# Performance work log

Hardware: AMD Instinct MI355X
Metric: run time of the kernel (lower is better)

Reference implementation:

```python
import jax, jax.numpy as jnp
import numpy as np

DIM = 768
HEADS = 12
HEAD_DIM = DIM // HEADS
HIDDEN = 4 * DIM


def layer_norm(x, g, b, eps=1e-5):
    mu = jnp.mean(x, axis=-1, keepdims=True)
    var = jnp.var(x, axis=-1, keepdims=True)
    return (x - mu) * jax.lax.rsqrt(var + eps) * g + b


def setup_inputs() -> dict:
    key = jax.random.key(0)
    ks = jax.random.split(key, 8)
    s = lambda fan_in: 1.0 / np.sqrt(fan_in)
    return {
        "x": jax.random.normal(ks[0], (16, 577, DIM), dtype=jnp.float32),
        "ln1_g": jnp.ones((DIM,), jnp.float32),
        "ln1_b": jnp.zeros((DIM,), jnp.float32),
        "w_qkv": jax.random.uniform(ks[1], (DIM, 3 * DIM), jnp.float32, -s(DIM), s(DIM)),
        "b_qkv": jnp.zeros((3 * DIM,), jnp.float32),
        "w_proj": jax.random.uniform(ks[2], (DIM, DIM), jnp.float32, -s(DIM), s(DIM)),
        "b_proj": jnp.zeros((DIM,), jnp.float32),
        "ln2_g": jnp.ones((DIM,), jnp.float32),
        "ln2_b": jnp.zeros((DIM,), jnp.float32),
        "w_fc1": jax.random.uniform(ks[3], (DIM, HIDDEN), jnp.float32, -s(DIM), s(DIM)),
        "b_fc1": jnp.zeros((HIDDEN,), jnp.float32),
        "w_fc2": jax.random.uniform(ks[4], (HIDDEN, DIM), jnp.float32, -s(HIDDEN), s(HIDDEN)),
        "b_fc2": jnp.zeros((DIM,), jnp.float32),
    }


def reference(x, ln1_g, ln1_b, w_qkv, b_qkv, w_proj, b_proj,
              ln2_g, ln2_b, w_fc1, b_fc1, w_fc2, b_fc2):
    B, N, C = x.shape
    scale = HEAD_DIM ** -0.5

    # --- attention branch (pre-norm) ---
    h = layer_norm(x, ln1_g, ln1_b)
    qkv = h @ w_qkv + b_qkv                               # [B,N,3C]
    qkv = qkv.reshape(B, N, 3, HEADS, HEAD_DIM)
    q, k, v = [qkv[:, :, i].transpose(0, 2, 1, 3) for i in range(3)]  # [B,H,N,D]
    attn = jnp.einsum("bhnd,bhmd->bhnm", q, k) * scale
    attn = jax.nn.softmax(attn, axis=-1)
    out = jnp.einsum("bhnm,bhmd->bhnd", attn, v)          # [B,H,N,D]
    out = out.transpose(0, 2, 1, 3).reshape(B, N, C)
    x = x + (out @ w_proj + b_proj)

    # --- MLP branch (pre-norm) ---
    h = layer_norm(x, ln2_g, ln2_b)
    h = jax.nn.gelu(h @ w_fc1 + b_fc1, approximate=False)
    x = x + (h @ w_fc2 + b_fc2)
    return x
```

## Files before the change

### kernel.cpp

```cpp
#include <hip/hip_runtime.h>
#include <hip/hip_bf16.h>
#include <math.h>

#define NB   16
#define NTOK 577
#define CDIM 768
#define NH   12
#define HID  3072
#define RTOT (NB*NTOK)
#define RPAD (((RTOT+127)/128)*128)
#define BH   (NB*NH)
#define QT   40
#define KF_C (CDIM/32)

typedef __attribute__((ext_vector_type(8))) short bf16x8;
typedef __attribute__((ext_vector_type(4))) float f32x4;
typedef unsigned short u16;

__device__ inline void load_lds16(const void* g, void* l) {
    __builtin_amdgcn_global_load_lds(
        (const __attribute__((address_space(1))) unsigned*)g,
        (__attribute__((address_space(3))) unsigned*)l, 16, 0, 0);
}

__device__ inline size_t blobA(int m, int c, int Kf) {
    return ((size_t)(m >> 4) * Kf + (c >> 5)) * 512 +
           (((c >> 3) & 3) * 16 + (m & 15)) * 8 + (c & 7);
}

__device__ inline float fast_gelu(float x) {
    float y = 0.7978845608f * (x + 0.044715f * x * x * x);
    float e = __expf(2.0f * y);
    float th = 1.0f - 2.0f / (e + 1.0f);
    return 0.5f * x * (1.0f + th);
}

__global__ __launch_bounds__(256) void wconvert_blob(
    const float* __restrict__ src, u16* __restrict__ dst, int K, int N)
{
    int n  = blockIdx.x * 256 + threadIdx.x;
    int kp = blockIdx.y;
    const float* s = src + (size_t)(kp * 8) * N + n;
    __hip_bfloat16 h0 = __float2bfloat16(s[0 * N]);
    __hip_bfloat16 h1 = __float2bfloat16(s[1 * N]);
    __hip_bfloat16 h2 = __float2bfloat16(s[2 * N]);
    __hip_bfloat16 h3 = __float2bfloat16(s[3 * N]);
    __hip_bfloat16 h4 = __float2bfloat16(s[4 * N]);
    __hip_bfloat16 h5 = __float2bfloat16(s[5 * N]);
    __hip_bfloat16 h6 = __float2bfloat16(s[6 * N]);
    __hip_bfloat16 h7 = __float2bfloat16(s[7 * N]);
    ushort4 a = make_ushort4(*(u16*)&h0, *(u16*)&h1, *(u16*)&h2, *(u16*)&h3);
    ushort4 b = make_ushort4(*(u16*)&h4, *(u16*)&h5, *(u16*)&h6, *(u16*)&h7);
    u16* d = dst + ((size_t)(n >> 4) * (K >> 5) + (kp >> 2)) * 512 +
             ((kp & 3) * 16 + (n & 15)) * 8;
    *(ushort4*)(d)     = a;
    *(ushort4*)(d + 4) = b;
}

__global__ __launch_bounds__(256) void ln_kernel(
    const float* __restrict__ x, const float* __restrict__ g,
    const float* __restrict__ b, u16* __restrict__ out)
{
    int row = blockIdx.x;
    const float* xr = x + (size_t)row * CDIM;
    int t = threadIdx.x;
    float v0 = xr[t], v1 = xr[t + 256], v2 = xr[t + 512];
    float s  = v0 + v1 + v2;
    float s2 = v0*v0 + v1*v1 + v2*v2;
    #pragma unroll
    for (int off = 32; off; off >>= 1) {
        s  += __shfl_xor(s, off);
        s2 += __shfl_xor(s2, off);
    }
    __shared__ float red[10];
    int wave = t >> 6, lane = t & 63;
    if (lane == 0) { red[wave] = s; red[wave + 4] = s2; }
    __syncthreads();
    if (t == 0) {
        float ts  = red[0] + red[1] + red[2] + red[3];
        float ts2 = red[4] + red[5] + red[6] + red[7];
        float mu  = ts * (1.0f / CDIM);
        float var = ts2 * (1.0f / CDIM) - mu * mu;
        red[8] = mu;
        red[9] = rsqrtf(var + 1e-5f);
    }
    __syncthreads();
    float mu = red[8], rs = red[9];
    #pragma unroll
    for (int i = 0; i < 3; ++i) {
        int c = t + i * 256;
        float v = (i == 0 ? v0 : (i == 1 ? v1 : v2));
        __hip_bfloat16 hb = __float2bfloat16((v - mu) * rs * g[c] + b[c]);
        out[blobA(row, c, KF_C)] = *(u16*)&hb;
    }
}

template<int TM>
__global__ __launch_bounds__(64) void flat_gemm(
    const u16* __restrict__ Ab, const u16* __restrict__ Bb,
    const float* __restrict__ bias, const float* __restrict__ res,
    void* __restrict__ outv,
    u16* __restrict__ Qp, u16* __restrict__ Kp, u16* __restrict__ Vp,
    int M, int Nc, int K, int nb, int mb, int flags)
{
    __shared__ u16 sb[TM * 1024];
    int lane = threadIdx.x & 63;
    int fr = lane & 15, fq = lane >> 4;

    int fid = blockIdx.x;
    int xcd = fid & 7, w = fid >> 3;
    int slab = w / nb, n = w - slab * nb;
    int m = slab * 8 + xcd;
    if (m >= mb) return;
    int m0 = m * (TM * 16), n0 = n * 64;

    int Kf = K >> 5;
    size_t tstr = (size_t)Kf * 512;
    const u16* Ap = Ab + (size_t)(m0 >> 4) * tstr + lane * 8;
    const u16* Bp = Bb + (size_t)(n0 >> 4) * tstr + lane * 8;

    f32x4 acc[TM][4];
    #pragma unroll
    for (int i = 0; i < TM; ++i)
        #pragma unroll
        for (int j = 0; j < 4; ++j) acc[i][j] = (f32x4){0.f, 0.f, 0.f, 0.f};

    bf16x8 af[TM], bf[4];
    #pragma unroll
    for (int tm = 0; tm < TM; ++tm) af[tm] = *(const bf16x8*)(Ap + tm * tstr);
    #pragma unroll
    for (int tn = 0; tn < 4; ++tn) bf[tn] = *(const bf16x8*)(Bp + tn * tstr);

    for (int kf = 0; kf < Kf; ++kf) {
        bf16x8 an[TM], bn[4];
        if (kf + 1 < Kf) {
            size_t o = (size_t)(kf + 1) * 512;
            #pragma unroll
            for (int tm = 0; tm < TM; ++tm)
                an[tm] = *(const bf16x8*)(Ap + tm * tstr + o);
            #pragma unroll
            for (int tn = 0; tn < 4; ++tn)
                bn[tn] = *(const bf16x8*)(Bp + tn * tstr + o);
        }
        #pragma unroll
        for (int tm = 0; tm < TM; ++tm)
            #pragma unroll
            for (int tn = 0; tn < 4; ++tn)
                acc[tm][tn] = __builtin_amdgcn_mfma_f32_16x16x32_bf16(
                    af[tm], bf[tn], acc[tm][tn], 0, 0, 0);
        #pragma unroll
        for (int i = 0; i < TM; ++i) af[i] = an[i];
        #pragma unroll
        for (int i = 0; i < 4; ++i)  bf[i] = bn[i];
    }

    float* outf = (float*)outv;
    u16* outblob = (u16*)outv;
    int gelu = flags & 1;
    int KfO = Nc >> 5;

    if (flags & 8) {
        int sec = n0 / CDIM;
        int h   = (n0 % CDIM) / 64;
        #pragma unroll
        for (int tm = 0; tm < TM; ++tm) {
            #pragma unroll
            for (int rg = 0; rg < 4; ++rg) {
                int gm = m0 + tm * 16 + fq * 4 + rg;
                if (gm >= M) continue;
                int b   = gm / NTOK;
                int row = gm - b * NTOK;
                int bh  = b * NH + h;
                #pragma unroll
                for (int tn = 0; tn < 4; ++tn) {
                    int d = tn * 16 + fr;
                    float v = acc[tm][tn][rg] + bias[n0 + tn * 16 + fr];
                    __hip_bfloat16 hb = __float2bfloat16(v);
                    if (sec == 0) {
                        Qp[(size_t)(bh * QT + (row >> 4)) * 1024 + (d >> 5) * 512 +
                           (((d >> 3) & 3) * 16 + (row & 15)) * 8 + (d & 7)] = *(u16*)&hb;
                    } else if (sec == 1) {
                        Kp[(size_t)(bh * QT + (row >> 4)) * 1024 + (d >> 5) * 512 +
                           (((d >> 3) & 3) * 16 + (row & 15)) * 8 + (d & 7)] = *(u16*)&hb;
                    } else {
                        Vp[((size_t)(bh * 4 + (d >> 4)) * 20 + (row >> 5)) * 512 +
                           (((row >> 3) & 3) * 16 + (d & 15)) * 8 + (row & 7)] = *(u16*)&hb;
                    }
                }
            }
        }
        return;
    }

    if (flags & 4) {
        #pragma unroll
        for (int tm = 0; tm < TM; ++tm)
            #pragma unroll
            for (int tn = 0; tn < 4; ++tn)
                #pragma unroll
                for (int rg = 0; rg < 4; ++rg) {
                    int cl = tn * 16 + fr;
                    float v = acc[tm][tn][rg] + bias[n0 + cl];
                    if (gelu) v = fast_gelu(v);
                    __hip_bfloat16 hb = __float2bfloat16(v);
                    sb[tm * 1024 + (cl >> 5) * 512 +
                       (((cl >> 3) & 3) * 16 + fq * 4 + rg) * 8 + (cl & 7)] = *(u16*)&hb;
                }
        #pragma unroll
        for (int tm = 0; tm < TM; ++tm) {
            u16* dst = outblob + ((size_t)((m0 >> 4) + tm) * KfO + (n0 >> 5)) * 512;
            *(bf16x8*)(dst + lane * 16)     = *(const bf16x8*)(sb + tm * 1024 + lane * 16);
            *(bf16x8*)(dst + lane * 16 + 8) = *(const bf16x8*)(sb + tm * 1024 + lane * 16 + 8);
        }
        return;
    }

    #pragma unroll
    for (int tm = 0; tm < TM; ++tm) {
        #pragma unroll
        for (int rg = 0; rg < 4; ++rg) {
            int gm = m0 + tm * 16 + fq * 4 + rg;
            if (gm >= M) continue;
            #pragma unroll
            for (int tn = 0; tn < 4; ++tn) {
                int gn = n0 + tn * 16 + fr;
                float v = acc[tm][tn][rg] + bias[gn];
                if (gelu) v = fast_gelu(v);
                if (res)  v += res[(size_t)gm * Nc + gn];
                outf[(size_t)gm * Nc + gn] = v;
            }
        }
    }
}

__global__ __launch_bounds__(256) void attn_mfma(
    const u16* __restrict__ Qp, const u16* __restrict__ Kp,
    const u16* __restrict__ Vp, u16* __restrict__ outp)
{
    __shared__ __align__(16) u16 Ks[4096];
    __shared__ __align__(16) u16 Vs[4096];
    __shared__ __align__(16) u16 Ps[4 * 16 * 72];

    int bh = blockIdx.y, qc = blockIdx.x;
    int b = bh / NH, h = bh % NH;
    int t = threadIdx.x, lane = t & 63, wv = t >> 6;
    int fr = lane & 15, fq = lane >> 4;

    int mt = qc * 4 + wv;
    const u16* qbase = Qp + (size_t)(bh * QT + mt) * 1024 + lane * 8;
    bf16x8 qf0 = *(const bf16x8*)(qbase);
    bf16x8 qf1 = *(const bf16x8*)(qbase + 512);

    const u16* kg = Kp + (size_t)bh * (QT * 1024) + wv * 1024 + lane * 8;
    const u16* vg = Vp + ((size_t)(bh * 4 + wv) * 20) * 512 + lane * 8;
    u16* lK  = Ks + wv * 1024;
    u16* lV  = Vs + wv * 1024;
    u16* psw = Ps + wv * (16 * 72);

    f32x4 o[4];
    float m_r[4], l_r[4];
    #pragma unroll
    for (int i = 0; i < 4; ++i) {
        o[i] = (f32x4){0.f, 0.f, 0.f, 0.f};
        m_r[i] = -1e30f; l_r[i] = 0.f;
    }

    for (int kt = 0; kt < 10; ++kt) {
        load_lds16(kg + kt * 4096,       lK);
        load_lds16(kg + kt * 4096 + 512, lK + 512);
        load_lds16(vg + kt * 1024,       lV);
        load_lds16(vg + kt * 1024 + 512, lV + 512);
        __syncthreads();

        f32x4 sc[4];
        #pragma unroll
        for (int nt = 0; nt < 4; ++nt) {
            sc[nt] = (f32x4){0.f, 0.f, 0.f, 0.f};
            bf16x8 kf0 = *(const bf16x8*)(Ks + (nt * 2 + 0) * 512 + lane * 8);
            bf16x8 kf1 = *(const bf16x8*)(Ks + (nt * 2 + 1) * 512 + lane * 8);
            sc[nt] = __builtin_amdgcn_mfma_f32_16x16x32_bf16(qf0, kf0, sc[nt], 0, 0, 0);
            sc[nt] = __builtin_amdgcn_mfma_f32_16x16x32_bf16(qf1, kf1, sc[nt], 0, 0, 0);
        }

        int j0 = kt * 64;
        float p[4][4], rm[4];
        #pragma unroll
        for (int rg = 0; rg < 4; ++rg) rm[rg] = -1e30f;
        #pragma unroll
        for (int nt = 0; nt < 4; ++nt) {
            bool valid = (j0 + nt * 16 + fr) < NTOK;
            #pragma unroll
            for (int rg = 0; rg < 4; ++rg) {
                float sv = valid ? sc[nt][rg] * 0.125f : -1e30f;
                p[nt][rg] = sv;
                rm[rg] = fmaxf(rm[rg], sv);
            }
        }
        #pragma unroll
        for (int rg = 0; rg < 4; ++rg) {
            #pragma unroll
            for (int off = 1; off < 16; off <<= 1)
                rm[rg] = fmaxf(rm[rg], __shfl_xor(rm[rg], off));
        }
        float alpha[4], rs[4];
        #pragma unroll
        for (int rg = 0; rg < 4; ++rg) {
            float mn = fmaxf(m_r[rg], rm[rg]);
            alpha[rg] = __expf(m_r[rg] - mn);
            m_r[rg] = mn;
            rs[rg] = 0.f;
        }
        #pragma unroll
        for (int nt = 0; nt < 4; ++nt)
            #pragma unroll
            for (int rg = 0; rg < 4; ++rg) {
                float pv = __expf(p[nt][rg] - m_r[rg]);
                p[nt][rg] = pv;
                rs[rg] += pv;
            }
        #pragma unroll
        for (int rg = 0; rg < 4; ++rg) {
            #pragma unroll
            for (int off = 1; off < 16; off <<= 1)
                rs[rg] += __shfl_xor(rs[rg], off);
            l_r[rg] = l_r[rg] * alpha[rg] + rs[rg];
        }

        #pragma unroll
        for (int nt = 0; nt < 4; ++nt)
            #pragma unroll
            for (int rg = 0; rg < 4; ++rg) {
                __hip_bfloat16 hb = __float2bfloat16(p[nt][rg]);
                psw[(fq * 4 + rg) * 72 + nt * 16 + fr] = *(u16*)&hb;
            }
        #pragma unroll
        for (int dt = 0; dt < 4; ++dt)
            #pragma unroll
            for (int rg = 0; rg < 4; ++rg)
                o[dt][rg] *= alpha[rg];

        bf16x8 pf0 = *(const bf16x8*)(psw + fr * 72 + fq * 8);
        bf16x8 pf1 = *(const bf16x8*)(psw + fr * 72 + 32 + fq * 8);
        #pragma unroll
        for (int dt = 0; dt < 4; ++dt) {
            bf16x8 bv0 = *(const bf16x8*)(Vs + (dt * 2 + 0) * 512 + lane * 8);
            bf16x8 bv1 = *(const bf16x8*)(Vs + (dt * 2 + 1) * 512 + lane * 8);
            o[dt] = __builtin_amdgcn_mfma_f32_16x16x32_bf16(pf0, bv0, o[dt], 0, 0, 0);
            o[dt] = __builtin_amdgcn_mfma_f32_16x16x32_bf16(pf1, bv1, o[dt], 0, 0, 0);
        }
        __syncthreads();
    }

    #pragma unroll
    for (int rg = 0; rg < 4; ++rg) {
        int row = qc * 64 + wv * 16 + fq * 4 + rg;
        if (row < NTOK) {
            float rl = 1.0f / l_r[rg];
            int grow = b * NTOK + row;
            #pragma unroll
            for (int dt = 0; dt < 4; ++dt) {
                __hip_bfloat16 hb = __float2bfloat16(o[dt][rg] * rl);
                outp[blobA(grow, h * 64 + dt * 16 + fr, KF_C)] = *(u16*)&hb;
            }
        }
    }
}

static inline int swz_grid(int nb, int mb) { return nb * (((mb + 7) / 8) * 8); }

extern "C" void kernel_launch(void* const* d_in, const int* in_sizes, int n_in,
                              void* d_out, int out_size, void* d_ws, size_t ws_size,
                              hipStream_t stream)
{
    const float* x      = (const float*)d_in[0];
    const float* ln1_g  = (const float*)d_in[1];
    const float* ln1_b  = (const float*)d_in[2];
    const float* w_qkv  = (const float*)d_in[3];
    const float* b_qkv  = (const float*)d_in[4];
    const float* w_proj = (const float*)d_in[5];
    const float* b_proj = (const float*)d_in[6];
    const float* ln2_g  = (const float*)d_in[7];
    const float* ln2_b  = (const float*)d_in[8];
    const float* w_fc1  = (const float*)d_in[9];
    const float* b_fc1  = (const float*)d_in[10];
    const float* w_fc2  = (const float*)d_in[11];
    const float* b_fc2  = (const float*)d_in[12];
    float* out = (float*)d_out;

    char* w = (char*)d_ws;
    u16* Bqkv = (u16*)w; w += (size_t)3*CDIM*CDIM*2;
    u16* Bproj= (u16*)w; w += (size_t)CDIM*CDIM*2;
    u16* Bfc1 = (u16*)w; w += (size_t)HID*CDIM*2;
    u16* Bfc2 = (u16*)w; w += (size_t)CDIM*HID*2;
    u16* hA   = (u16*)w; w += (size_t)RPAD*CDIM*2;
    u16* h3A  = (u16*)w; w += (size_t)RPAD*HID*2;
    u16* Qp   = (u16*)w; w += (size_t)BH*QT*1024*2;
    u16* Kp   = (u16*)w; w += (size_t)BH*QT*1024*2;
    u16* Vp   = (u16*)w; w += (size_t)BH*4*20*512*2;

    int mb4 = (RTOT + 63) / 64;

    wconvert_blob<<<dim3(3*CDIM/256, CDIM/8), 256, 0, stream>>>(w_qkv,  Bqkv, CDIM, 3*CDIM);
    wconvert_blob<<<dim3(CDIM/256,   CDIM/8), 256, 0, stream>>>(w_proj, Bproj, CDIM, CDIM);
    wconvert_blob<<<dim3(HID/256,    CDIM/8), 256, 0, stream>>>(w_fc1,  Bfc1, CDIM, HID);
    wconvert_blob<<<dim3(CDIM/256,   HID/8),  256, 0, stream>>>(w_fc2,  Bfc2, HID, CDIM);

    ln_kernel<<<RTOT, 256, 0, stream>>>(x, ln1_g, ln1_b, hA);
    flat_gemm<4><<<swz_grid(3*CDIM/64, mb4), 64, 0, stream>>>(
        hA, Bqkv, b_qkv, nullptr, nullptr, Qp, Kp, Vp,
        RTOT, 3*CDIM, CDIM, 3*CDIM/64, mb4, 8);
    attn_mfma<<<dim3(10, BH), 256, 0, stream>>>(Qp, Kp, Vp, hA);
    flat_gemm<4><<<swz_grid(CDIM/64, mb4), 64, 0, stream>>>(
        hA, Bproj, b_proj, x, out, nullptr, nullptr, nullptr,
        RTOT, CDIM, CDIM, CDIM/64, mb4, 0);
    ln_kernel<<<RTOT, 256, 0, stream>>>(out, ln2_g, ln2_b, hA);
    flat_gemm<4><<<swz_grid(HID/64, mb4), 64, 0, stream>>>(
        hA, Bfc1, b_fc1, nullptr, h3A, nullptr, nullptr, nullptr,
        RTOT, HID, CDIM, HID/64, mb4, 1 | 4);
    flat_gemm<4><<<swz_grid(CDIM/64, mb4), 64, 0, stream>>>(
        h3A, Bfc2, b_fc2, out, out, nullptr, nullptr, nullptr,
        RTOT, CDIM, HID, CDIM/64, mb4, 0);
}
```

Baseline: 486.0 us.

## Replace single-wave register GEMM with 4-wave LDS-staged double-buffered tile GEMM

Replaces the one-wavefront GEMM that streamed A and B fragments straight from global memory into registers with a 256-thread kernel. Each block stages a larger tile (128x128 or 64x128) into LDS via global_load_lds with double buffering, and four waves share it as a 2x2 layout. This raises reuse of loaded A/B data across waves and cuts redundant global traffic. The cost is a block-wide barrier per K step and no XCD-aware block swizzle. Flags become template parameters, and the gelu branch in the fp32 epilogue is dropped.

```diff
diff --git a/kernel.cpp b/kernel.cpp
--- a/kernel.cpp
+++ b/kernel.cpp
@@ -95,86 +95,92 @@
     }
 }
 
-template<int TM>
-__global__ __launch_bounds__(64) void flat_gemm(
+template<int MBL, int NBL, int FLAGS>
+__global__ __launch_bounds__(256) void tile_gemm(
     const u16* __restrict__ Ab, const u16* __restrict__ Bb,
     const float* __restrict__ bias, const float* __restrict__ res,
     void* __restrict__ outv,
     u16* __restrict__ Qp, u16* __restrict__ Kp, u16* __restrict__ Vp,
-    int M, int Nc, int K, int nb, int mb, int flags)
+    int M, int Nc, int K)
 {
-    __shared__ u16 sb[TM * 1024];
-    int lane = threadIdx.x & 63;
+    constexpr int NST  = (MBL + NBL) / 4;
+    constexpr int BUFU = (MBL + NBL) * 512;
+    constexpr int MH2  = MBL / 2, NW2 = NBL / 2;
+    __shared__ __align__(16) u16 smem[2 * BUFU];
+
+    int tid = threadIdx.x, lane = tid & 63, wv = tid >> 6;
     int fr = lane & 15, fq = lane >> 4;
-
-    int fid = blockIdx.x;
-    int xcd = fid & 7, w = fid >> 3;
-    int slab = w / nb, n = w - slab * nb;
-    int m = slab * 8 + xcd;
-    if (m >= mb) return;
-    int m0 = m * (TM * 16), n0 = n * 64;
-
+    int wm = wv >> 1, wn = wv & 1;
+
+    int m0 = blockIdx.y * (MBL * 16), n0 = blockIdx.x * (NBL * 16);
     int Kf = K >> 5;
     size_t tstr = (size_t)Kf * 512;
-    const u16* Ap = Ab + (size_t)(m0 >> 4) * tstr + lane * 8;
-    const u16* Bp = Bb + (size_t)(n0 >> 4) * tstr + lane * 8;
-
-    f32x4 acc[TM][4];
-    #pragma unroll
-    for (int i = 0; i < TM; ++i)
-        #pragma unroll
-        for (int j = 0; j < 4; ++j) acc[i][j] = (f32x4){0.f, 0.f, 0.f, 0.f};
-
-    bf16x8 af[TM], bf[4];
-    #pragma unroll
-    for (int tm = 0; tm < TM; ++tm) af[tm] = *(const bf16x8*)(Ap + tm * tstr);
-    #pragma unroll
-    for (int tn = 0; tn < 4; ++tn) bf[tn] = *(const bf16x8*)(Bp + tn * tstr);
-
-    for (int kf = 0; kf < Kf; ++kf) {
-        bf16x8 an[TM], bn[4];
-        if (kf + 1 < Kf) {
-            size_t o = (size_t)(kf + 1) * 512;
-            #pragma unroll
-            for (int tm = 0; tm < TM; ++tm)
-                an[tm] = *(const bf16x8*)(Ap + tm * tstr + o);
-            #pragma unroll
-            for (int tn = 0; tn < 4; ++tn)
-                bn[tn] = *(const bf16x8*)(Bp + tn * tstr + o);
-        }
-        #pragma unroll
-        for (int tm = 0; tm < TM; ++tm)
-            #pragma unroll
-            for (int tn = 0; tn < 4; ++tn)
-                acc[tm][tn] = __builtin_amdgcn_mfma_f32_16x16x32_bf16(
-                    af[tm], bf[tn], acc[tm][tn], 0, 0, 0);
-        #pragma unroll
-        for (int i = 0; i < TM; ++i) af[i] = an[i];
-        #pragma unroll
-        for (int i = 0; i < 4; ++i)  bf[i] = bn[i];
-    }
-
+
+    const u16* gp[NST];
+    u16* ldst[NST];
+    #pragma unroll
+    for (int i = 0; i < NST; ++i) {
+        int bi = wv + i * 4;
+        gp[i] = (bi < MBL)
+            ? Ab + ((size_t)(m0 >> 4) + bi) * tstr + lane * 8
+            : Bb + ((size_t)(n0 >> 4) + (bi - MBL)) * tstr + lane * 8;
+        ldst[i] = smem + bi * 512;
+    }
+
+    f32x4 acc[MH2][NW2];
+    #pragma unroll
+    for (int mi = 0; mi < MH2; ++mi)
+        #pragma unroll
+        for (int ni = 0; ni < NW2; ++ni) acc[mi][ni] = (f32x4){0.f, 0.f, 0.f, 0.f};
+
+    #pragma unroll
+    for (int i = 0; i < NST; ++i) load_lds16(gp[i], ldst[i]);
+    __syncthreads();
+
+    for (int t = 0; t < Kf; ++t) {
+        int cur = (t & 1) * BUFU, nxt = ((t + 1) & 1) * BUFU;
+        if (t + 1 < Kf) {
+            #pragma unroll
+            for (int i = 0; i < NST; ++i)
+                load_lds16(gp[i] + (size_t)(t + 1) * 512, ldst[i] + nxt);
+        }
+        bf16x8 a[MH2], bfr[NW2];
+        #pragma unroll
+        for (int mi = 0; mi < MH2; ++mi)
+            a[mi] = *(const bf16x8*)(smem + cur + (wm * MH2 + mi) * 512 + lane * 8);
+        #pragma unroll
+        for (int ni = 0; ni < NW2; ++ni)
+            bfr[ni] = *(const bf16x8*)(smem + cur + (MBL + wn * NW2 + ni) * 512 + lane * 8);
+        #pragma unroll
+        for (int mi = 0; mi < MH2; ++mi)
+            #pragma unroll
+            for (int ni = 0; ni < NW2; ++ni)
+                acc[mi][ni] = __builtin_amdgcn_mfma_f32_16x16x32_bf16(
+                    a[mi], bfr[ni], acc[mi][ni], 0, 0, 0);
+        __syncthreads();
+    }
+
+    int m0w = m0 + wm * (MH2 * 16);
+    int n0w = n0 + wn * (NW2 * 16);
     float* outf = (float*)outv;
     u16* outblob = (u16*)outv;
-    int gelu = flags & 1;
-    int KfO = Nc >> 5;
-
-    if (flags & 8) {
-        int sec = n0 / CDIM;
-        int h   = (n0 % CDIM) / 64;
-        #pragma unroll
-        for (int tm = 0; tm < TM; ++tm) {
+
+    if constexpr ((FLAGS & 8) != 0) {
+        int sec = n0w / CDIM;
+        int h   = (n0w % CDIM) / 64;
+        #pragma unroll
+        for (int mi = 0; mi < MH2; ++mi) {
             #pragma unroll
             for (int rg = 0; rg < 4; ++rg) {
-                int gm = m0 + tm * 16 + fq * 4 + rg;
+                int gm = m0w + mi * 16 + fq * 4 + rg;
                 if (gm >= M) continue;
                 int b   = gm / NTOK;
                 int row = gm - b * NTOK;
                 int bh  = b * NH + h;
                 #pragma unroll
-                for (int tn = 0; tn < 4; ++tn) {
-                    int d = tn * 16 + fr;
-                    float v = acc[tm][tn][rg] + bias[n0 + tn * 16 + fr];
+                for (int ni = 0; ni < NW2; ++ni) {
+                    int d = ni * 16 + fr;
+                    float v = acc[mi][ni][rg] + bias[n0w + d];
                     __hip_bfloat16 hb = __float2bfloat16(v);
                     if (sec == 0) {
                         Qp[(size_t)(bh * QT + (row >> 4)) * 1024 + (d >> 5) * 512 +
@@ -192,41 +198,40 @@
         return;
     }
 
-    if (flags & 4) {
-        #pragma unroll
-        for (int tm = 0; tm < TM; ++tm)
-            #pragma unroll
-            for (int tn = 0; tn < 4; ++tn)
+    if constexpr ((FLAGS & 4) != 0) {
+        u16* sb = smem + wv * 1024;
+        int KfO = Nc >> 5;
+        #pragma unroll
+        for (int mi = 0; mi < MH2; ++mi) {
+            #pragma unroll
+            for (int ni = 0; ni < NW2; ++ni)
                 #pragma unroll
                 for (int rg = 0; rg < 4; ++rg) {
-                    int cl = tn * 16 + fr;
-                    float v = acc[tm][tn][rg] + bias[n0 + cl];
-                    if (gelu) v = fast_gelu(v);
+                    int cl = ni * 16 + fr;
+                    float v = acc[mi][ni][rg] + bias[n0w + cl];
+                    if (FLAGS & 1) v = fast_gelu(v);
                     __hip_bfloat16 hb = __float2bfloat16(v);
-                    sb[tm * 1024 + (cl >> 5) * 512 +
+                    sb[(cl >> 5) * 512 +
                        (((cl >> 3) & 3) * 16 + fq * 4 + rg) * 8 + (cl & 7)] = *(u16*)&hb;
                 }
-        #pragma unroll
-        for (int tm = 0; tm < TM; ++tm) {
-            u16* dst = outblob + ((size_t)((m0 >> 4) + tm) * KfO + (n0 >> 5)) * 512;
-            *(bf16x8*)(dst + lane * 16)     = *(const bf16x8*)(sb + tm * 1024 + lane * 16);
-            *(bf16x8*)(dst + lane * 16 + 8) = *(const bf16x8*)(sb + tm * 1024 + lane * 16 + 8);
+            u16* dst = outblob + ((size_t)((m0w >> 4) + mi) * KfO + (n0w >> 5)) * 512;
+            *(bf16x8*)(dst + lane * 16)     = *(const bf16x8*)(sb + lane * 16);
+            *(bf16x8*)(dst + lane * 16 + 8) = *(const bf16x8*)(sb + lane * 16 + 8);
         }
         return;
     }
 
     #pragma unroll
-    for (int tm = 0; tm < TM; ++tm) {
+    for (int mi = 0; mi < MH2; ++mi) {
         #pragma unroll
         for (int rg = 0; rg < 4; ++rg) {
-            int gm = m0 + tm * 16 + fq * 4 + rg;
+            int gm = m0w + mi * 16 + fq * 4 + rg;
             if (gm >= M) continue;
             #pragma unroll
-            for (int tn = 0; tn < 4; ++tn) {
-                int gn = n0 + tn * 16 + fr;
-                float v = acc[tm][tn][rg] + bias[gn];
-                if (gelu) v = fast_gelu(v);
-                if (res)  v += res[(size_t)gm * Nc + gn];
+            for (int ni = 0; ni < NW2; ++ni) {
+                int gn = n0w + ni * 16 + fr;
+                float v = acc[mi][ni][rg] + bias[gn];
+                if (res) v += res[(size_t)gm * Nc + gn];
                 outf[(size_t)gm * Nc + gn] = v;
             }
         }
@@ -365,8 +370,6 @@
         }
     }
 }
-
-static inline int swz_grid(int nb, int mb) { return nb * (((mb + 7) / 8) * 8); }
 
 extern "C" void kernel_launch(void* const* d_in, const int* in_sizes, int n_in,
                               void* d_out, int out_size, void* d_ws, size_t ws_size,
@@ -398,7 +401,8 @@
     u16* Kp   = (u16*)w; w += (size_t)BH*QT*1024*2;
     u16* Vp   = (u16*)w; w += (size_t)BH*4*20*512*2;
 
-    int mb4 = (RTOT + 63) / 64;
+    int mt128 = (RTOT + 127) / 128;
+    int mt64  = (RTOT + 63) / 64;
 
     wconvert_blob<<<dim3(3*CDIM/256, CDIM/8), 256, 0, stream>>>(w_qkv,  Bqkv, CDIM, 3*CDIM);
     wconvert_blob<<<dim3(CDIM/256,   CDIM/8), 256, 0, stream>>>(w_proj, Bproj, CDIM, CDIM);
@@ -406,18 +410,14 @@
     wconvert_blob<<<dim3(CDIM/256,   HID/8),  256, 0, stream>>>(w_fc2,  Bfc2, HID, CDIM);
 
     ln_kernel<<<RTOT, 256, 0, stream>>>(x, ln1_g, ln1_b, hA);
-    flat_gemm<4><<<swz_grid(3*CDIM/64, mb4), 64, 0, stream>>>(
-        hA, Bqkv, b_qkv, nullptr, nullptr, Qp, Kp, Vp,
-        RTOT, 3*CDIM, CDIM, 3*CDIM/64, mb4, 8);
+    tile_gemm<8, 8, 8><<<dim3(3*CDIM/128, mt128), 256, 0, stream>>>(
+        hA, Bqkv, b_qkv, nullptr, nullptr, Qp, Kp, Vp, RTOT, 3*CDIM, CDIM);
     attn_mfma<<<dim3(10, BH), 256, 0, stream>>>(Qp, Kp, Vp, hA);
-    flat_gemm<4><<<swz_grid(CDIM/64, mb4), 64, 0, stream>>>(
-        hA, Bproj, b_proj, x, out, nullptr, nullptr, nullptr,
-        RTOT, CDIM, CDIM, CDIM/64, mb4, 0);
+    tile_gemm<4, 8, 0><<<dim3(CDIM/128, mt64), 256, 0, stream>>>(
+        hA, Bproj, b_proj, x, out, nullptr, nullptr, nullptr, RTOT, CDIM, CDIM);
     ln_kernel<<<RTOT, 256, 0, stream>>>(out, ln2_g, ln2_b, hA);
-    flat_gemm<4><<<swz_grid(HID/64, mb4), 64, 0, stream>>>(
-        hA, Bfc1, b_fc1, nullptr, h3A, nullptr, nullptr, nullptr,
-        RTOT, HID, CDIM, HID/64, mb4, 1 | 4);
-    flat_gemm<4><<<swz_grid(CDIM/64, mb4), 64, 0, stream>>>(
-        h3A, Bfc2, b_fc2, out, out, nullptr, nullptr, nullptr,
-        RTOT, CDIM, HID, CDIM/64, mb4, 0);
-}
+    tile_gemm<8, 8, 5><<<dim3(HID/128, mt128), 256, 0, stream>>>(
+        hA, Bfc1, b_fc1, nullptr, h3A, nullptr, nullptr, nullptr, RTOT, HID, CDIM);
+    tile_gemm<4, 8, 0><<<dim3(CDIM/128, mt64), 256, 0, stream>>>(
+        h3A, Bfc2, b_fc2, out, out, nullptr, nullptr, nullptr, RTOT, CDIM, HID);
+}
```

Result: no change. 480.1 us (-1.2%).
